# Optimization experiments

Hardware: AMD Instinct MI355X
Metric: run time of the kernel (lower is better)

## Reference

```python
import jax, jax.numpy as jnp
import numpy as np
import math

D_MODEL = 1024
NUM_HEADS = 16
HEAD_DIM = D_MODEL // NUM_HEADS
BLOCK_SIZE = 64
THRESHOLD = 0.99


def setup_inputs() -> dict:
    key = jax.random.key(0)
    ks = jax.random.split(key, 12)
    B, S, D = 2, 2048, D_MODEL
    scale = 1.0 / math.sqrt(D)
    x = jax.random.normal(ks[0], (B, S, D), dtype=jnp.float32)
    G_ii = jax.random.uniform(ks[1], (B, S), dtype=jnp.float32)
    # Linear weights stored as [in, out]; applied as x @ W + b (matches nn.Linear math).
    Wq = jax.random.normal(ks[2], (D, D), dtype=jnp.float32) * scale
    bq = jnp.zeros((D,), dtype=jnp.float32)
    Wk = jax.random.normal(ks[3], (D, D), dtype=jnp.float32) * scale
    bk = jnp.zeros((D,), dtype=jnp.float32)
    Wv = jax.random.normal(ks[4], (D, D), dtype=jnp.float32) * scale
    bv = jnp.zeros((D,), dtype=jnp.float32)
    Wo = jax.random.normal(ks[5], (D, D), dtype=jnp.float32) * scale
    bo = jnp.zeros((D,), dtype=jnp.float32)
    return {"x": x, "G_ii": G_ii, "Wq": Wq, "bq": bq, "Wk": Wk, "bk": bk,
            "Wv": Wv, "bv": bv, "Wo": Wo, "bo": bo}


def reference(x, G_ii, Wq, bq, Wk, bk, Wv, bv, Wo, bo):
    B, S, D = x.shape
    H, hd, bs = NUM_HEADS, HEAD_DIM, BLOCK_SIZE
    nb = S // bs

    # Projections and head split: [B, H, S, hd]
    q = (x @ Wq + bq).reshape(B, S, H, hd).transpose(0, 2, 1, 3)
    k = (x @ Wk + bk).reshape(B, S, H, hd).transpose(0, 2, 1, 3)
    v = (x @ Wv + bv).reshape(B, S, H, hd).transpose(0, 2, 1, 3)

    # Per-query-block scattering energy keep mask: block kept iff max |G_ii| >= threshold
    energy = jnp.abs(G_ii)                              # [B, S]
    block_max = energy.reshape(B, nb, bs).max(axis=-1)  # [B, nb]
    keep = (block_max >= THRESHOLD)                     # [B, nb] bool
    row_keep = jnp.repeat(keep, bs, axis=1)             # [B, S]

    # Kept query blocks attend densely (non-causal) over all keys; skipped blocks output zero.
    scores = jnp.einsum('bhqd,bhkd->bhqk', q, k) / math.sqrt(hd)  # [B, H, S, S]
    attn = jax.nn.softmax(scores, axis=-1)
    out = jnp.einsum('bhqk,bhkd->bhqd', attn, v)                  # [B, H, S, hd]
    out = out * row_keep[:, None, :, None].astype(out.dtype)

    out = out.transpose(0, 2, 1, 3).reshape(B, S, D)
    return out @ Wo + bo
```

## Files before the change

kernel.cpp:

```cpp
#include <hip/hip_runtime.h>
#include <math.h>

#define D_MODEL   1024
#define NUM_HEADS 16
#define HEAD_DIM  64
#define BS        64
#define NB        32
#define S_LEN     2048
#define BATCH     2
#define M_ROWS    (BATCH * S_LEN)
#define THRESH    0.99f
#define SCEXP     0.18033688f
#define NPH       (BATCH * NB * NUM_HEADS)
#define SPLITK    4

typedef __attribute__((ext_vector_type(8))) short bf16x8;
typedef __attribute__((ext_vector_type(8))) _Float16 f16x8;
typedef __attribute__((ext_vector_type(2))) __fp16 fp16v2;
typedef __attribute__((ext_vector_type(4))) float f32x4;

__device__ __forceinline__ unsigned short f2bf(float f) {
    unsigned int u = __float_as_uint(f);
    u += 0x7fff + ((u >> 16) & 1);
    return (unsigned short)(u >> 16);
}

__device__ __forceinline__ unsigned int pkrtz(float a, float b) {
    fp16v2 r = __builtin_amdgcn_cvt_pkrtz(a, b);
    return __builtin_bit_cast(unsigned int, r);
}

__device__ __forceinline__ void gload16(const void* gptr, void* lptr) {
    __builtin_amdgcn_global_load_lds(
        (const __attribute__((address_space(1))) void*)gptr,
        (__attribute__((address_space(3))) void*)lptr, 16, 0, 0);
}

__global__ __launch_bounds__(256) void prep_kernel(
    const float* __restrict__ x, const float* __restrict__ G,
    const float* __restrict__ Wq, const float* __restrict__ Wk,
    const float* __restrict__ Wv, const float* __restrict__ Wo,
    unsigned short* __restrict__ xb, unsigned short* __restrict__ wcat,
    unsigned short* __restrict__ wot, int* __restrict__ keep, int* __restrict__ work)
{
    const int bid = blockIdx.x, tid = threadIdx.x;
    __shared__ float T[64][65];

    if (bid < 2048) {
        size_t i = ((size_t)bid * 256 + tid) * 8;
        float4 a = *(const float4*)(x + i);
        float4 b = *(const float4*)(x + i + 4);
        uint4 o;
        o.x = (unsigned int)f2bf(a.x) | ((unsigned int)f2bf(a.y) << 16);
        o.y = (unsigned int)f2bf(a.z) | ((unsigned int)f2bf(a.w) << 16);
        o.z = (unsigned int)f2bf(b.x) | ((unsigned int)f2bf(b.y) << 16);
        o.w = (unsigned int)f2bf(b.z) | ((unsigned int)f2bf(b.w) << 16);
        *(uint4*)(xb + i) = o;
    } else if (bid < 3072) {
        int i = bid - 2048;
        int mat = i >> 8, rem = i & 255;
        int k0 = (rem & 15) * 64, n0 = (rem >> 4) * 64;
        const float* W = (mat == 0) ? Wq : (mat == 1) ? Wk : (mat == 2) ? Wv : Wo;
        int rr = tid >> 4, c4 = (tid & 15) * 4;
        #pragma unroll
        for (int j = 0; j < 4; j++) {
            int row = rr + j * 16;
            float4 v = *(const float4*)(W + (size_t)(k0 + row) * 1024 + n0 + c4);
            T[row][c4 + 0] = v.x; T[row][c4 + 1] = v.y;
            T[row][c4 + 2] = v.z; T[row][c4 + 3] = v.w;
        }
        __syncthreads();
        unsigned short* dst = (mat < 3) ? (wcat + (size_t)mat * 1024 * 1024) : wot;
        #pragma unroll
        for (int j = 0; j < 4; j++) {
            int n = rr + j * 16;
            unsigned int lo = (unsigned int)f2bf(T[c4 + 0][n]) | ((unsigned int)f2bf(T[c4 + 1][n]) << 16);
            unsigned int hi = (unsigned int)f2bf(T[c4 + 2][n]) | ((unsigned int)f2bf(T[c4 + 3][n]) << 16);
            *(uint2*)(dst + (size_t)(n0 + n) * 1024 + k0 + c4) = make_uint2(lo, hi);
        }
    } else {
        if (tid < 64) {
            int t = tid;
            const float4* g = (const float4*)(G + (size_t)t * 64);
            float mx = 0.f;
            #pragma unroll
            for (int j = 0; j < 16; j++) {
                float4 v = g[j];
                mx = fmaxf(mx, fmaxf(fmaxf(fabsf(v.x), fabsf(v.y)), fmaxf(fabsf(v.z), fabsf(v.w))));
            }
            bool k = (mx >= THRESH);
            unsigned long long bal = __ballot(k);
            int nk = __popcll(bal);
            unsigned long long below = bal & ((1ull << t) - 1ull);
            int nbelow = (int)__popcll(below);
            keep[t] = k ? 1 : 0;
            if (t == 0) work[0] = nk;
            int pos = k ? nbelow : (nk + t - nbelow);
            work[1 + pos] = t;
        }
    }
}

__global__ __launch_bounds__(256, 3) void gemm_qkv(
    const unsigned short* __restrict__ A, const unsigned short* __restrict__ Bt,
    const float* __restrict__ bq, const float* __restrict__ bk, const float* __restrict__ bv,
    const int* __restrict__ keep, unsigned short* __restrict__ qk, unsigned short* __restrict__ vt)
{
    const int n0 = blockIdx.x * 128, m0 = blockIdx.y * 128;
    const int tid = threadIdx.x, w = tid >> 6, lane = tid & 63;
    const int quad = lane >> 4, l16 = lane & 15;
    const int wm = w >> 1, wn = w & 1;
    const int kindb = n0 >> 10;
    if (kindb == 0 && !(keep[2 * blockIdx.y] | keep[2 * blockIdx.y + 1])) return;

    __shared__ union {
        struct { unsigned short As[2][128 * 32]; unsigned short Bs[2][128 * 32]; } s;
        unsigned short qkr[128 * 136];
        unsigned short vr[128 * 136];
    } u;

    f32x4 acc[4][4];
    #pragma unroll
    for (int mt = 0; mt < 4; mt++)
        #pragma unroll
        for (int nt = 0; nt < 4; nt++) acc[mt][nt] = (f32x4){0.f, 0.f, 0.f, 0.f};

    #define QSTAGE(it_, p_)                                                             \
        {                                                                               \
            int k0_ = (it_) * 32;                                                       \
            _Pragma("unroll")                                                           \
            for (int j = 0; j < 2; j++) {                                               \
                int s_ = w * 128 + j * 64 + lane; int row = s_ >> 2, cl = s_ & 3;       \
                int c = cl ^ ((row >> 1) & 3);                                          \
                gload16(A + (size_t)(m0 + row) * 1024 + k0_ + c * 8,                    \
                        &u.s.As[p_][(w * 128 + j * 64) * 8]);                           \
            }                                                                           \
            _Pragma("unroll")                                                           \
            for (int j = 0; j < 2; j++) {                                               \
                int s_ = w * 128 + j * 64 + lane; int row = s_ >> 2, cl = s_ & 3;       \
                int c = cl ^ ((row >> 1) & 3);                                          \
                gload16(Bt + (size_t)(n0 + row) * 1024 + k0_ + c * 8,                   \
                        &u.s.Bs[p_][(w * 128 + j * 64) * 8]);                           \
            }                                                                           \
        }

    QSTAGE(0, 0)

    for (int it = 0; it < 32; it++) {
        const int p = it & 1;
        __syncthreads();
        if (it + 1 < 32) QSTAGE(it + 1, (it + 1) & 1)

        bf16x8 af[4], bfr[4];
        #pragma unroll
        for (int mt = 0; mt < 4; mt++) {
            int row = wm * 64 + mt * 16 + l16;
            int cl = quad ^ ((row >> 1) & 3);
            af[mt] = *(const bf16x8*)&u.s.As[p][(row * 4 + cl) * 8];
        }
        #pragma unroll
        for (int nt = 0; nt < 4; nt++) {
            int row = wn * 64 + nt * 16 + l16;
            int cl = quad ^ ((row >> 1) & 3);
            bfr[nt] = *(const bf16x8*)&u.s.Bs[p][(row * 4 + cl) * 8];
        }
        #pragma unroll
        for (int mt = 0; mt < 4; mt++)
            #pragma unroll
            for (int nt = 0; nt < 4; nt++)
                acc[mt][nt] = __builtin_amdgcn_mfma_f32_16x16x32_bf16(af[mt], bfr[nt], acc[mt][nt], 0, 0, 0);
    }
    __syncthreads();

    if (kindb < 2) {
        const float* bp = (kindb == 0) ? bq : bk;
        const float sc = (kindb == 0) ? SCEXP : 1.0f;
        #pragma unroll
        for (int nt = 0; nt < 4; nt++) {
            int coll = wn * 64 + nt * 16 + l16;
            float bb = bp[(n0 & 1023) + coll];
            #pragma unroll
            for (int mt = 0; mt < 4; mt++)
                #pragma unroll
                for (int r = 0; r < 4; r++) {
                    int row = wm * 64 + mt * 16 + quad * 4 + r;
                    u.qkr[row * 136 + coll] = f2bf((acc[mt][nt][r] + bb) * sc);
                }
        }
        __syncthreads();
        #pragma unroll
        for (int i = 0; i < 8; i++) {
            int s_ = tid + i * 256;
            int row = s_ >> 4, c16 = s_ & 15;
            uint4 v = *(const uint4*)&u.qkr[row * 136 + c16 * 8];
            *(uint4*)(qk + (size_t)(m0 + row) * 2048 + n0 + c16 * 8) = v;
        }
    } else {
        #pragma unroll
        for (int nt = 0; nt < 4; nt++) {
            int coll = wn * 64 + nt * 16 + l16;
            float bb = bv[(n0 - 2048) + coll];
            #pragma unroll
            for (int mt = 0; mt < 4; mt++) {
                int s0 = wm * 64 + mt * 16 + quad * 4;
                uint2 pv;
                pv.x = pkrtz(acc[mt][nt][0] + bb, acc[mt][nt][1] + bb);
                pv.y = pkrtz(acc[mt][nt][2] + bb, acc[mt][nt][3] + bb);
                *(uint2*)&u.vr[coll * 136 + s0] = pv;
            }
        }
        __syncthreads();
        const int b_ = m0 >> 11, sbase = m0 & 2047;
        #pragma unroll
        for (int i = 0; i < 8; i++) {
            int s_ = tid + i * 256;
            int coll = s_ >> 4, ch = s_ & 15;
            uint4 v = *(const uint4*)&u.vr[coll * 136 + ch * 8];
            int colg = n0 - 2048 + coll;
            int h_ = colg >> 6, d = colg & 63;
            *(uint4*)(vt + ((size_t)(b_ * NUM_HEADS + h_) * HEAD_DIM + d) * 2048 + sbase + ch * 8) = v;
        }
    }
}

__global__ __launch_bounds__(256, 4) void gemm_out(
    const unsigned short* __restrict__ A, const unsigned short* __restrict__ Bt,
    const float* __restrict__ bo, const int* __restrict__ keep, float* __restrict__ out)
{
    const int n0 = blockIdx.x * 64, m0 = blockIdx.y * 64;
    const int tid = threadIdx.x, w = tid >> 6, lane = tid & 63;
    const int quad = lane >> 4, l16 = lane & 15;
    const int wm = w >> 1, wn = w & 1;

    if (!keep[blockIdx.y]) {
        #pragma unroll
        for (int i = 0; i < 4; i++) {
            int s_ = tid + i * 256;
            int row = s_ >> 4, c = (s_ & 15) * 4;
            *(float4*)(out + (size_t)(m0 + row) * 1024 + n0 + c) = *(const float4*)(bo + n0 + c);
        }
        return;
    }

    __shared__ unsigned short Asl[2][64 * 32];
    __shared__ unsigned short Bsl[2][64 * 32];

    f32x4 acc[2][2];
    #pragma unroll
    for (int mt = 0; mt < 2; mt++)
        #pragma unroll
        for (int nt = 0; nt < 2; nt++) acc[mt][nt] = (f32x4){0.f, 0.f, 0.f, 0.f};

    #define OSTAGE(it_, p_)                                                             \
        {                                                                               \
            int k0_ = (it_) * 32;                                                       \
            int s_ = w * 64 + lane; int row = s_ >> 2, cl = s_ & 3;                     \
            int c = cl ^ ((row >> 1) & 3);                                              \
            gload16(A  + (size_t)(m0 + row) * 1024 + k0_ + c * 8, &Asl[p_][(w * 64) * 8]); \
            gload16(Bt + (size_t)(n0 + row) * 1024 + k0_ + c * 8, &Bsl[p_][(w * 64) * 8]); \
        }

    OSTAGE(0, 0)

    for (int it = 0; it < 32; it++) {
        const int p = it & 1;
        __syncthreads();
        if (it + 1 < 32) OSTAGE(it + 1, (it + 1) & 1)

        bf16x8 af[2], bfr[2];
        #pragma unroll
        for (int mt = 0; mt < 2; mt++) {
            int row = wm * 32 + mt * 16 + l16;
            int cl = quad ^ ((row >> 1) & 3);
            af[mt] = *(const bf16x8*)&Asl[p][(row * 4 + cl) * 8];
        }
        #pragma unroll
        for (int nt = 0; nt < 2; nt++) {
            int row = wn * 32 + nt * 16 + l16;
            int cl = quad ^ ((row >> 1) & 3);
            bfr[nt] = *(const bf16x8*)&Bsl[p][(row * 4 + cl) * 8];
        }
        #pragma unroll
        for (int mt = 0; mt < 2; mt++)
            #pragma unroll
            for (int nt = 0; nt < 2; nt++)
                acc[mt][nt] = __builtin_amdgcn_mfma_f32_16x16x32_bf16(af[mt], bfr[nt], acc[mt][nt], 0, 0, 0);
    }

    #pragma unroll
    for (int nt = 0; nt < 2; nt++) {
        int col = n0 + wn * 32 + nt * 16 + l16;
        float bb = bo[col];
        #pragma unroll
        for (int mt = 0; mt < 2; mt++) {
            int mb = m0 + wm * 32 + mt * 16 + quad * 4;
            #pragma unroll
            for (int r = 0; r < 4; r++)
                out[(size_t)(mb + r) * 1024 + col] = acc[mt][nt][r] + bb;
        }
    }
}

__global__ __launch_bounds__(256, 4) void attn_kernel(
    const unsigned short* __restrict__ qk, const unsigned short* __restrict__ Vtg,
    const int* __restrict__ work,
    unsigned short* __restrict__ opart, float* __restrict__ lpart)
{
    const int bx = blockIdx.x, half = blockIdx.y;
    const int pair = bx >> 4, h = bx & 15;
    const int tid  = threadIdx.x;
    const int w    = tid >> 6, lane = tid & 63;
    const int quad = lane >> 4, l16 = lane & 15;

    if (pair >= work[0]) return;
    const int e = work[1 + pair];
    const int b = e >> 5, qblk = e & 31;

    __shared__ unsigned short Kbuf[2][BS * HEAD_DIM];
    __shared__ unsigned short Vbuf[2][HEAD_DIM * BS];
    __shared__ unsigned short Pt[4][16 * 64];

    const int KEYS = S_LEN / SPLITK;
    const int NCH  = KEYS / BS;
    const unsigned short* Qb = qk + (size_t)(b * S_LEN) * 2048 + h * 64;
    const unsigned short* Kb = qk + (size_t)(b * S_LEN + half * KEYS) * 2048 + 1024 + h * 64;
    const unsigned short* Vb = Vtg + (size_t)(b * NUM_HEADS + h) * HEAD_DIM * 2048 + half * KEYS;

    const int qrow = qblk * BS + w * 16 + l16;
    bf16x8 qf[2];
    #pragma unroll
    for (int ks = 0; ks < 2; ks++)
        qf[ks] = *(const bf16x8*)(Qb + (size_t)qrow * 2048 + ks * 32 + quad * 8);

    f32x4 o[4];
    #pragma unroll
    for (int mt = 0; mt < 4; mt++) o[mt] = (f32x4){0.f, 0.f, 0.f, 0.f};
    float l = 0.f;

    const int sA = w * 128 + lane, sB = sA + 64;
    const int rA = sA >> 3, cA = (sA & 7) ^ (rA & 7);
    const int rB = sB >> 3, cB = (sB & 7) ^ (rB & 7);
    const size_t koA = (size_t)rA * 2048 + cA * 8, koB = (size_t)rB * 2048 + cB * 8;

    uint4 kr0, kr1, vr0, vr1;
    #define LOADREGS(kc_)                                                       \
        {                                                                       \
            const unsigned short* kg_ = Kb + (size_t)(kc_) * BS * 2048;         \
            const unsigned short* vg_ = Vb + (size_t)(kc_) * BS;                \
            kr0 = *(const uint4*)(kg_ + koA); kr1 = *(const uint4*)(kg_ + koB); \
            vr0 = *(const uint4*)(vg_ + koA); vr1 = *(const uint4*)(vg_ + koB); \
        }
    #define WRITELDS(pb_)                                                       \
        {                                                                       \
            *(uint4*)&Kbuf[pb_][(size_t)sA * 8] = kr0;                          \
            *(uint4*)&Kbuf[pb_][(size_t)sB * 8] = kr1;                          \
            *(uint4*)&Vbuf[pb_][(size_t)sA * 8] = vr0;                          \
            *(uint4*)&Vbuf[pb_][(size_t)sB * 8] = vr1;                          \
        }

    LOADREGS(0)
    WRITELDS(0)
    __syncthreads();

    #pragma unroll
    for (int kc = 0; kc < NCH; kc++) {
        const int p = kc & 1;
        if (kc + 1 < NCH) LOADREGS(kc + 1)

        f32x4 st[4];
        #pragma unroll
        for (int mt = 0; mt < 4; mt++) {
            f32x4 acc = {0.f, 0.f, 0.f, 0.f};
            #pragma unroll
            for (int ks = 0; ks < 2; ks++) {
                int kk = mt * 16 + l16;
                bf16x8 kf = *(const bf16x8*)&Kbuf[p][(size_t)(kk * 8 + ((ks * 4 + quad) ^ (kk & 7))) * 8];
                acc = __builtin_amdgcn_mfma_f32_16x16x32_bf16(kf, qf[ks], acc, 0, 0, 0);
            }
            st[mt] = acc;
        }

        float pv[16], sum = 0.f;
        #pragma unroll
        for (int mt = 0; mt < 4; mt++)
            #pragma unroll
            for (int r = 0; r < 4; r++) {
                float ex = exp2f(st[mt][r]);
                pv[mt * 4 + r] = ex; sum += ex;
            }
        sum += __shfl_xor(sum, 16, 64);
        sum += __shfl_xor(sum, 32, 64);
        l += sum;

        #pragma unroll
        for (int mt = 0; mt < 4; mt++) {
            unsigned int lo = pkrtz(pv[mt * 4 + 0], pv[mt * 4 + 1]);
            unsigned int hi = pkrtz(pv[mt * 4 + 2], pv[mt * 4 + 3]);
            int c16 = 2 * mt + (quad >> 1);
            *(uint2*)&Pt[w][l16 * 64 + ((c16 ^ (l16 & 7)) * 8 + (quad & 1) * 4)] = make_uint2(lo, hi);
        }

        #pragma unroll
        for (int ks = 0; ks < 2; ks++) {
            f16x8 pf = *(const f16x8*)&Pt[w][l16 * 64 + (((4 * ks + quad) ^ (l16 & 7)) * 8)];
            #pragma unroll
            for (int mt = 0; mt < 4; mt++) {
                int d = mt * 16 + l16;
                f16x8 vf = *(const f16x8*)&Vbuf[p][(size_t)(d * 8 + ((ks * 4 + quad) ^ (d & 7))) * 8];
                o[mt] = __builtin_amdgcn_mfma_f32_16x16x32_f16(vf, pf, o[mt], 0, 0, 0);
            }
        }

        if (kc + 1 < NCH) {
            WRITELDS(p ^ 1)
            __syncthreads();
        }
    }

    unsigned short* ob = opart + ((size_t)(half * NPH + bx)) * 4096 + tid * 16;
    uint4 w0, w1;
    w0.x = pkrtz(o[0][0], o[0][1]); w0.y = pkrtz(o[0][2], o[0][3]);
    w0.z = pkrtz(o[1][0], o[1][1]); w0.w = pkrtz(o[1][2], o[1][3]);
    w1.x = pkrtz(o[2][0], o[2][1]); w1.y = pkrtz(o[2][2], o[2][3]);
    w1.z = pkrtz(o[3][0], o[3][1]); w1.w = pkrtz(o[3][2], o[3][3]);
    *(uint4*)ob = w0;
    *(uint4*)(ob + 8) = w1;
    if (quad == 0) lpart[(size_t)(half * NPH + bx) * 64 + w * 16 + l16] = l;
}

__global__ __launch_bounds__(256) void attn_combine(
    const unsigned short* __restrict__ opart, const float* __restrict__ lpart,
    const int* __restrict__ work, unsigned short* __restrict__ attn_out)
{
    const int bx = blockIdx.x;
    const int pair = bx >> 4, h = bx & 15;
    const int tid  = threadIdx.x;
    const int w    = tid >> 6, lane = tid & 63;
    const int quad = lane >> 4, l16 = lane & 15;

    const int e = work[1 + pair];
    const int b = e >> 5, qblk = e & 31;
    unsigned short* ablk = attn_out + ((size_t)(b * S_LEN + qblk * BS)) * D_MODEL + h * HEAD_DIM;

    if (pair >= work[0]) {
        uint4 z = make_uint4(0, 0, 0, 0);
        #pragma unroll
        for (int i = 0; i < 2; i++) {
            int u = tid + i * 256;
            int row = u >> 3, c8 = (u & 7) * 8;
            *(uint4*)(ablk + (size_t)row * D_MODEL + c8) = z;
        }
        return;
    }

    __shared__ float Obuf[4][HEAD_DIM * 17];

    float osum[16];
    #pragma unroll
    for (int j = 0; j < 16; j++) osum[j] = 0.f;
    float lsum = 0.f;
    #pragma unroll
    for (int hf = 0; hf < SPLITK; hf++) {
        const f16x8* pp = (const f16x8*)(opart + ((size_t)hf * NPH + bx) * 4096 + tid * 16);
        f16x8 a0 = pp[0], a1 = pp[1];
        #pragma unroll
        for (int j = 0; j < 8; j++) {
            osum[j]     += (float)a0[j];
            osum[8 + j] += (float)a1[j];
        }
        lsum += lpart[((size_t)hf * NPH + bx) * 64 + w * 16 + l16];
    }
    float inv = 1.0f / lsum;

    #pragma unroll
    for (int mt = 0; mt < 4; mt++)
        #pragma unroll
        for (int r = 0; r < 4; r++)
            Obuf[w][(mt * 16 + quad * 4 + r) * 17 + l16] = osum[mt * 4 + r] * inv;
    #pragma unroll
    for (int i = 0; i < 4; i++) {
        int uu = lane + 64 * i;
        int row = uu >> 4, d4 = (uu & 15) * 4;
        float x0 = Obuf[w][(d4 + 0) * 17 + row];
        float x1 = Obuf[w][(d4 + 1) * 17 + row];
        float x2 = Obuf[w][(d4 + 2) * 17 + row];
        float x3 = Obuf[w][(d4 + 3) * 17 + row];
        unsigned int lo = (unsigned int)f2bf(x0) | ((unsigned int)f2bf(x1) << 16);
        unsigned int hi = (unsigned int)f2bf(x2) | ((unsigned int)f2bf(x3) << 16);
        *(uint2*)(ablk + (size_t)(w * 16 + row) * D_MODEL + d4) = make_uint2(lo, hi);
    }
}

extern "C" void kernel_launch(void* const* d_in, const int* in_sizes, int n_in,
                              void* d_out, int out_size, void* d_ws, size_t ws_size,
                              hipStream_t stream) {
    const float* x  = (const float*)d_in[0];
    const float* G  = (const float*)d_in[1];
    const float* Wq = (const float*)d_in[2];
    const float* bq = (const float*)d_in[3];
    const float* Wk = (const float*)d_in[4];
    const float* bk = (const float*)d_in[5];
    const float* Wv = (const float*)d_in[6];
    const float* bv = (const float*)d_in[7];
    const float* Wo = (const float*)d_in[8];
    const float* bo = (const float*)d_in[9];
    float* out = (float*)d_out;

    char* wsp = (char*)d_ws;
    int* keep = (int*)wsp;
    int* work = keep + 64;
    unsigned short* xb    = (unsigned short*)(wsp + 1024);
    unsigned short* wcat  = xb + (size_t)M_ROWS * D_MODEL;
    unsigned short* wot   = wcat + (size_t)3 * 1024 * 1024;
    unsigned short* qk    = wot + (size_t)1024 * 1024;
    unsigned short* vt    = qk + (size_t)M_ROWS * 2048;
    unsigned short* attnb = vt + (size_t)BATCH * NUM_HEADS * HEAD_DIM * 2048;
    unsigned short* opart = attnb + (size_t)M_ROWS * D_MODEL;
    float* lpart = (float*)(opart + (size_t)SPLITK * NPH * 4096);

    prep_kernel<<<3073, 256, 0, stream>>>(x, G, Wq, Wk, Wv, Wo, xb, wcat, wot, keep, work);

    gemm_qkv<<<dim3(3072 / 128, M_ROWS / 128), 256, 0, stream>>>(
        xb, wcat, bq, bk, bv, keep, qk, vt);

    attn_kernel<<<dim3(NPH, SPLITK), 256, 0, stream>>>(qk, vt, work, opart, lpart);
    attn_combine<<<NPH, 256, 0, stream>>>(opart, lpart, work, attnb);

    gemm_out<<<dim3(1024 / 64, M_ROWS / 64), 256, 0, stream>>>(attnb, wot, bo, keep, out);
}
```

Measured before the change: 186.3 us.

## Software-pipeline QK^T one chunk ahead of softmax-PV in attention kernel

Restructures the attention inner loop so the QK^T MFMA for chunk i+1 is issued before the softmax and PV for chunk i. K and V loads and LDS writes are staggered separately so K runs two chunks ahead and V one chunk ahead. The change also adds s_setprio around the MFMA sections and swaps exp2f for the raw hardware exp2 builtin. The aim is to overlap exp and softmax ALU work with matrix-core work and to hide global load latency, at the cost of more live registers for the second score buffer.

```diff
diff --git a/kernel.cpp b/kernel.cpp
--- a/kernel.cpp
+++ b/kernel.cpp
@@ -343,79 +343,100 @@
     const size_t koA = (size_t)rA * 2048 + cA * 8, koB = (size_t)rB * 2048 + cB * 8;
 
     uint4 kr0, kr1, vr0, vr1;
-    #define LOADREGS(kc_)                                                       \
+    #define LOADK(kc_)                                                          \
         {                                                                       \
             const unsigned short* kg_ = Kb + (size_t)(kc_) * BS * 2048;         \
+            kr0 = *(const uint4*)(kg_ + koA); kr1 = *(const uint4*)(kg_ + koB); \
+        }
+    #define LOADV(kc_)                                                          \
+        {                                                                       \
             const unsigned short* vg_ = Vb + (size_t)(kc_) * BS;                \
-            kr0 = *(const uint4*)(kg_ + koA); kr1 = *(const uint4*)(kg_ + koB); \
             vr0 = *(const uint4*)(vg_ + koA); vr1 = *(const uint4*)(vg_ + koB); \
         }
-    #define WRITELDS(pb_)                                                       \
+    #define WRITEK(pb_)                                                         \
         {                                                                       \
             *(uint4*)&Kbuf[pb_][(size_t)sA * 8] = kr0;                          \
             *(uint4*)&Kbuf[pb_][(size_t)sB * 8] = kr1;                          \
+        }
+    #define WRITEV(pb_)                                                         \
+        {                                                                       \
             *(uint4*)&Vbuf[pb_][(size_t)sA * 8] = vr0;                          \
             *(uint4*)&Vbuf[pb_][(size_t)sB * 8] = vr1;                          \
         }
-
-    LOADREGS(0)
-    WRITELDS(0)
+    #define QKT(pb_, st_)                                                                        \
+        {                                                                                        \
+            __builtin_amdgcn_s_setprio(1);                                                       \
+            _Pragma("unroll")                                                                    \
+            for (int mt = 0; mt < 4; mt++) {                                                     \
+                f32x4 a_ = {0.f, 0.f, 0.f, 0.f};                                                 \
+                _Pragma("unroll")                                                                \
+                for (int ks = 0; ks < 2; ks++) {                                                 \
+                    int kk = mt * 16 + l16;                                                      \
+                    bf16x8 kf = *(const bf16x8*)&Kbuf[pb_][(size_t)(kk * 8 + ((ks * 4 + quad) ^ (kk & 7))) * 8]; \
+                    a_ = __builtin_amdgcn_mfma_f32_16x16x32_bf16(kf, qf[ks], a_, 0, 0, 0);       \
+                }                                                                                \
+                st_[mt] = a_;                                                                    \
+            }                                                                                    \
+            __builtin_amdgcn_s_setprio(0);                                                       \
+        }
+    #define SMPV(st_, pbv_)                                                                      \
+        {                                                                                        \
+            float pvv[16], sum = 0.f;                                                            \
+            _Pragma("unroll")                                                                    \
+            for (int mt = 0; mt < 4; mt++)                                                       \
+                _Pragma("unroll")                                                                \
+                for (int r = 0; r < 4; r++) {                                                    \
+                    float ex = __builtin_amdgcn_exp2f(st_[mt][r]);                               \
+                    pvv[mt * 4 + r] = ex; sum += ex;                                             \
+                }                                                                                \
+            sum += __shfl_xor(sum, 16, 64);                                                      \
+            sum += __shfl_xor(sum, 32, 64);                                                      \
+            l += sum;                                                                            \
+            _Pragma("unroll")                                                                    \
+            for (int mt = 0; mt < 4; mt++) {                                                     \
+                unsigned int lo = pkrtz(pvv[mt * 4 + 0], pvv[mt * 4 + 1]);                       \
+                unsigned int hi = pkrtz(pvv[mt * 4 + 2], pvv[mt * 4 + 3]);                       \
+                int c16 = 2 * mt + (quad >> 1);                                                  \
+                *(uint2*)&Pt[w][l16 * 64 + ((c16 ^ (l16 & 7)) * 8 + (quad & 1) * 4)] = make_uint2(lo, hi); \
+            }                                                                                    \
+            __builtin_amdgcn_s_setprio(1);                                                       \
+            _Pragma("unroll")                                                                    \
+            for (int ks = 0; ks < 2; ks++) {                                                     \
+                f16x8 pf = *(const f16x8*)&Pt[w][l16 * 64 + (((4 * ks + quad) ^ (l16 & 7)) * 8)];\
+                _Pragma("unroll")                                                                \
+                for (int mt = 0; mt < 4; mt++) {                                                 \
+                    int d = mt * 16 + l16;                                                       \
+                    f16x8 vf = *(const f16x8*)&Vbuf[pbv_][(size_t)(d * 8 + ((ks * 4 + quad) ^ (d & 7))) * 8]; \
+                    o[mt] = __builtin_amdgcn_mfma_f32_16x16x32_f16(vf, pf, o[mt], 0, 0, 0);      \
+                }                                                                                \
+            }                                                                                    \
+            __builtin_amdgcn_s_setprio(0);                                                       \
+        }
+
+    LOADK(0) LOADV(0)
+    WRITEK(0) WRITEV(0)
+    LOADK(1)
     __syncthreads();
 
-    #pragma unroll
-    for (int kc = 0; kc < NCH; kc++) {
-        const int p = kc & 1;
-        if (kc + 1 < NCH) LOADREGS(kc + 1)
-
-        f32x4 st[4];
-        #pragma unroll
-        for (int mt = 0; mt < 4; mt++) {
-            f32x4 acc = {0.f, 0.f, 0.f, 0.f};
-            #pragma unroll
-            for (int ks = 0; ks < 2; ks++) {
-                int kk = mt * 16 + l16;
-                bf16x8 kf = *(const bf16x8*)&Kbuf[p][(size_t)(kk * 8 + ((ks * 4 + quad) ^ (kk & 7))) * 8];
-                acc = __builtin_amdgcn_mfma_f32_16x16x32_bf16(kf, qf[ks], acc, 0, 0, 0);
-            }
-            st[mt] = acc;
-        }
-
-        float pv[16], sum = 0.f;
-        #pragma unroll
-        for (int mt = 0; mt < 4; mt++)
-            #pragma unroll
-            for (int r = 0; r < 4; r++) {
-                float ex = exp2f(st[mt][r]);
-                pv[mt * 4 + r] = ex; sum += ex;
-            }
-        sum += __shfl_xor(sum, 16, 64);
-        sum += __shfl_xor(sum, 32, 64);
-        l += sum;
-
-        #pragma unroll
-        for (int mt = 0; mt < 4; mt++) {
-            unsigned int lo = pkrtz(pv[mt * 4 + 0], pv[mt * 4 + 1]);
-            unsigned int hi = pkrtz(pv[mt * 4 + 2], pv[mt * 4 + 3]);
-            int c16 = 2 * mt + (quad >> 1);
-            *(uint2*)&Pt[w][l16 * 64 + ((c16 ^ (l16 & 7)) * 8 + (quad & 1) * 4)] = make_uint2(lo, hi);
-        }
-
-        #pragma unroll
-        for (int ks = 0; ks < 2; ks++) {
-            f16x8 pf = *(const f16x8*)&Pt[w][l16 * 64 + (((4 * ks + quad) ^ (l16 & 7)) * 8)];
-            #pragma unroll
-            for (int mt = 0; mt < 4; mt++) {
-                int d = mt * 16 + l16;
-                f16x8 vf = *(const f16x8*)&Vbuf[p][(size_t)(d * 8 + ((ks * 4 + quad) ^ (d & 7))) * 8];
-                o[mt] = __builtin_amdgcn_mfma_f32_16x16x32_f16(vf, pf, o[mt], 0, 0, 0);
-            }
-        }
-
-        if (kc + 1 < NCH) {
-            WRITELDS(p ^ 1)
-            __syncthreads();
-        }
-    }
+    f32x4 st0[4], st1[4];
+    QKT(0, st0)
+    WRITEK(1)
+    LOADK(2) LOADV(1)
+    __syncthreads();
+
+    #pragma unroll
+    for (int i = 0; i < NCH - 1; i++) {
+        QKT((i + 1) & 1, st1)
+        SMPV(st0, i & 1)
+        if (i + 2 < NCH) WRITEK(i & 1)
+        WRITEV((i + 1) & 1)
+        if (i + 3 < NCH) LOADK(i + 3)
+        if (i + 2 < NCH) LOADV(i + 2)
+        __syncthreads();
+        #pragma unroll
+        for (int mt = 0; mt < 4; mt++) st0[mt] = st1[mt];
+    }
+    SMPV(st0, (NCH - 1) & 1)
 
     unsigned short* ob = opart + ((size_t)(half * NPH + bx)) * 4096 + tid * 16;
     uint4 w0, w1;
```

After: 191.7 us. +2.9%, slower.

## Process two kept query blocks per attention workgroup to share K/V tiles

Applied to the files above, without the earlier changes.

The work list is rebuilt so kept query blocks are paired within each batch, padded with a duplicate when the count is odd, and skipped and dummy slots are flagged. Each attention workgroup now computes two query blocks against the same staged K/V chunk, halving K/V global loads and LDS staging per query block and doubling MFMA work per load. It also uses the raw exp2 intrinsic and raises wave priority around the MFMA sections. The cost is more registers (occupancy hint lowered from 4 to 3), wasted work on padded pairs, and more complex slot indexing in the combine kernel.

```diff
diff --git a/kernel.cpp b/kernel.cpp
--- a/kernel.cpp
+++ b/kernel.cpp
@@ -11,8 +11,9 @@
 #define M_ROWS    (BATCH * S_LEN)
 #define THRESH    0.99f
 #define SCEXP     0.18033688f
-#define NPH       (BATCH * NB * NUM_HEADS)
 #define SPLITK    4
+#define NSLOT     66
+#define SLOTB     (NSLOT * 16)
 
 typedef __attribute__((ext_vector_type(8))) short bf16x8;
 typedef __attribute__((ext_vector_type(8))) _Float16 f16x8;
@@ -90,13 +91,27 @@
             }
             bool k = (mx >= THRESH);
             unsigned long long bal = __ballot(k);
-            int nk = __popcll(bal);
-            unsigned long long below = bal & ((1ull << t) - 1ull);
-            int nbelow = (int)__popcll(below);
+            unsigned int mk0 = (unsigned int)bal, mk1 = (unsigned int)(bal >> 32);
+            int nk0 = __popc(mk0), nk1 = __popc(mk1);
+            int ND0 = (nk0 + 1) >> 1, ND1 = (nk1 + 1) >> 1;
             keep[t] = k ? 1 : 0;
-            if (t == 0) work[0] = nk;
-            int pos = k ? nbelow : (nk + t - nbelow);
-            work[1 + pos] = t;
+            int tb = t & 31, bb = t >> 5;
+            unsigned int mb = bb ? mk1 : mk0;
+            unsigned int msk = (tb == 0) ? 0u : ((1u << tb) - 1u);
+            int rank = __popc(mb & msk);
+            int rd   = __popc(~mb & msk);
+            int base = bb ? 2 * ND0 : 0;
+            int dbase = 2 * ND0 + 2 * ND1;
+            int doff = bb ? (32 - nk0) : 0;
+            if (k)  work[1 + base + rank] = t;
+            else    work[1 + dbase + doff + rd] = t | (1 << 8);
+            if (t == 0) {
+                work[0] = ND0 + ND1;
+                if (nk0 & 1) work[1 + nk0] = (31 - __clz(mk0)) | (2 << 8);
+                if (nk1 & 1) work[1 + 2 * ND0 + nk1] = (63 - __clz(mk1)) | (2 << 8);
+                int total = dbase + (64 - nk0 - nk1);
+                for (int j = total; j < NSLOT; j++) work[1 + j] = (2 << 8);
+            }
         }
     }
 }
@@ -301,24 +316,25 @@
     }
 }
 
-__global__ __launch_bounds__(256, 4) void attn_kernel(
+__global__ __launch_bounds__(256, 3) void attn_kernel(
     const unsigned short* __restrict__ qk, const unsigned short* __restrict__ Vtg,
     const int* __restrict__ work,
     unsigned short* __restrict__ opart, float* __restrict__ lpart)
 {
     const int bx = blockIdx.x, half = blockIdx.y;
-    const int pair = bx >> 4, h = bx & 15;
+    const int dpair = bx >> 4, h = bx & 15;
     const int tid  = threadIdx.x;
     const int w    = tid >> 6, lane = tid & 63;
     const int quad = lane >> 4, l16 = lane & 15;
 
-    if (pair >= work[0]) return;
-    const int e = work[1 + pair];
-    const int b = e >> 5, qblk = e & 31;
+    if (dpair >= work[0]) return;
+    const int j0 = 2 * dpair, j1 = j0 + 1;
+    const int t0 = work[1 + j0] & 63, t1 = work[1 + j1] & 63;
+    const int b = t0 >> 5, qb0 = t0 & 31, qb1 = t1 & 31;
 
     __shared__ unsigned short Kbuf[2][BS * HEAD_DIM];
     __shared__ unsigned short Vbuf[2][HEAD_DIM * BS];
-    __shared__ unsigned short Pt[4][16 * 64];
+    __shared__ unsigned short Pt[4][2][16 * 64];
 
     const int KEYS = S_LEN / SPLITK;
     const int NCH  = KEYS / BS;
@@ -326,16 +342,19 @@
     const unsigned short* Kb = qk + (size_t)(b * S_LEN + half * KEYS) * 2048 + 1024 + h * 64;
     const unsigned short* Vb = Vtg + (size_t)(b * NUM_HEADS + h) * HEAD_DIM * 2048 + half * KEYS;
 
-    const int qrow = qblk * BS + w * 16 + l16;
-    bf16x8 qf[2];
-    #pragma unroll
-    for (int ks = 0; ks < 2; ks++)
-        qf[ks] = *(const bf16x8*)(Qb + (size_t)qrow * 2048 + ks * 32 + quad * 8);
-
-    f32x4 o[4];
-    #pragma unroll
-    for (int mt = 0; mt < 4; mt++) o[mt] = (f32x4){0.f, 0.f, 0.f, 0.f};
-    float l = 0.f;
+    const int qrow0 = qb0 * BS + w * 16 + l16;
+    const int qrow1 = qb1 * BS + w * 16 + l16;
+    bf16x8 qf0[2], qf1[2];
+    #pragma unroll
+    for (int ks = 0; ks < 2; ks++) {
+        qf0[ks] = *(const bf16x8*)(Qb + (size_t)qrow0 * 2048 + ks * 32 + quad * 8);
+        qf1[ks] = *(const bf16x8*)(Qb + (size_t)qrow1 * 2048 + ks * 32 + quad * 8);
+    }
+
+    f32x4 o0[4], o1[4];
+    #pragma unroll
+    for (int mt = 0; mt < 4; mt++) { o0[mt] = (f32x4){0.f,0.f,0.f,0.f}; o1[mt] = (f32x4){0.f,0.f,0.f,0.f}; }
+    float l0 = 0.f, l1 = 0.f;
 
     const int sA = w * 128 + lane, sB = sA + 64;
     const int rA = sA >> 3, cA = (sA & 7) ^ (rA & 7);
@@ -367,49 +386,61 @@
         const int p = kc & 1;
         if (kc + 1 < NCH) LOADREGS(kc + 1)
 
-        f32x4 st[4];
+        f32x4 st0[4], st1[4];
+        __builtin_amdgcn_s_setprio(1);
         #pragma unroll
         for (int mt = 0; mt < 4; mt++) {
-            f32x4 acc = {0.f, 0.f, 0.f, 0.f};
+            f32x4 a0 = {0.f,0.f,0.f,0.f}, a1 = {0.f,0.f,0.f,0.f};
             #pragma unroll
             for (int ks = 0; ks < 2; ks++) {
                 int kk = mt * 16 + l16;
                 bf16x8 kf = *(const bf16x8*)&Kbuf[p][(size_t)(kk * 8 + ((ks * 4 + quad) ^ (kk & 7))) * 8];
-                acc = __builtin_amdgcn_mfma_f32_16x16x32_bf16(kf, qf[ks], acc, 0, 0, 0);
+                a0 = __builtin_amdgcn_mfma_f32_16x16x32_bf16(kf, qf0[ks], a0, 0, 0, 0);
+                a1 = __builtin_amdgcn_mfma_f32_16x16x32_bf16(kf, qf1[ks], a1, 0, 0, 0);
             }
-            st[mt] = acc;
-        }
-
-        float pv[16], sum = 0.f;
-        #pragma unroll
-        for (int mt = 0; mt < 4; mt++)
-            #pragma unroll
-            for (int r = 0; r < 4; r++) {
-                float ex = exp2f(st[mt][r]);
-                pv[mt * 4 + r] = ex; sum += ex;
-            }
-        sum += __shfl_xor(sum, 16, 64);
-        sum += __shfl_xor(sum, 32, 64);
-        l += sum;
-
+            st0[mt] = a0; st1[mt] = a1;
+        }
+        __builtin_amdgcn_s_setprio(0);
+
+        float sum0 = 0.f, sum1 = 0.f;
         #pragma unroll
         for (int mt = 0; mt < 4; mt++) {
-            unsigned int lo = pkrtz(pv[mt * 4 + 0], pv[mt * 4 + 1]);
-            unsigned int hi = pkrtz(pv[mt * 4 + 2], pv[mt * 4 + 3]);
             int c16 = 2 * mt + (quad >> 1);
-            *(uint2*)&Pt[w][l16 * 64 + ((c16 ^ (l16 & 7)) * 8 + (quad & 1) * 4)] = make_uint2(lo, hi);
-        }
-
+            int off = (c16 ^ (l16 & 7)) * 8 + (quad & 1) * 4;
+            float e00 = __builtin_amdgcn_exp2f(st0[mt][0]);
+            float e01 = __builtin_amdgcn_exp2f(st0[mt][1]);
+            float e02 = __builtin_amdgcn_exp2f(st0[mt][2]);
+            float e03 = __builtin_amdgcn_exp2f(st0[mt][3]);
+            sum0 += (e00 + e01) + (e02 + e03);
+            *(uint2*)&Pt[w][0][l16 * 64 + off] = make_uint2(pkrtz(e00, e01), pkrtz(e02, e03));
+            float e10 = __builtin_amdgcn_exp2f(st1[mt][0]);
+            float e11 = __builtin_amdgcn_exp2f(st1[mt][1]);
+            float e12 = __builtin_amdgcn_exp2f(st1[mt][2]);
+            float e13 = __builtin_amdgcn_exp2f(st1[mt][3]);
+            sum1 += (e10 + e11) + (e12 + e13);
+            *(uint2*)&Pt[w][1][l16 * 64 + off] = make_uint2(pkrtz(e10, e11), pkrtz(e12, e13));
+        }
+        sum0 += __shfl_xor(sum0, 16, 64);
+        sum0 += __shfl_xor(sum0, 32, 64);
+        sum1 += __shfl_xor(sum1, 16, 64);
+        sum1 += __shfl_xor(sum1, 32, 64);
+        l0 += sum0; l1 += sum1;
+
+        __builtin_amdgcn_s_setprio(1);
         #pragma unroll
         for (int ks = 0; ks < 2; ks++) {
-            f16x8 pf = *(const f16x8*)&Pt[w][l16 * 64 + (((4 * ks + quad) ^ (l16 & 7)) * 8)];
+            int poff = ((4 * ks + quad) ^ (l16 & 7)) * 8;
+            f16x8 pf0 = *(const f16x8*)&Pt[w][0][l16 * 64 + poff];
+            f16x8 pf1 = *(const f16x8*)&Pt[w][1][l16 * 64 + poff];
             #pragma unroll
             for (int mt = 0; mt < 4; mt++) {
                 int d = mt * 16 + l16;
                 f16x8 vf = *(const f16x8*)&Vbuf[p][(size_t)(d * 8 + ((ks * 4 + quad) ^ (d & 7))) * 8];
-                o[mt] = __builtin_amdgcn_mfma_f32_16x16x32_f16(vf, pf, o[mt], 0, 0, 0);
+                o0[mt] = __builtin_amdgcn_mfma_f32_16x16x32_f16(vf, pf0, o0[mt], 0, 0, 0);
+                o1[mt] = __builtin_amdgcn_mfma_f32_16x16x32_f16(vf, pf1, o1[mt], 0, 0, 0);
             }
         }
+        __builtin_amdgcn_s_setprio(0);
 
         if (kc + 1 < NCH) {
             WRITELDS(p ^ 1)
@@ -417,15 +448,30 @@
         }
     }
 
-    unsigned short* ob = opart + ((size_t)(half * NPH + bx)) * 4096 + tid * 16;
-    uint4 w0, w1;
-    w0.x = pkrtz(o[0][0], o[0][1]); w0.y = pkrtz(o[0][2], o[0][3]);
-    w0.z = pkrtz(o[1][0], o[1][1]); w0.w = pkrtz(o[1][2], o[1][3]);
-    w1.x = pkrtz(o[2][0], o[2][1]); w1.y = pkrtz(o[2][2], o[2][3]);
-    w1.z = pkrtz(o[3][0], o[3][1]); w1.w = pkrtz(o[3][2], o[3][3]);
-    *(uint4*)ob = w0;
-    *(uint4*)(ob + 8) = w1;
-    if (quad == 0) lpart[(size_t)(half * NPH + bx) * 64 + w * 16 + l16] = l;
+    {
+        unsigned short* ob = opart + ((size_t)(half * SLOTB + j0 * 16 + h)) * 4096 + tid * 16;
+        uint4 w0, w1;
+        w0.x = pkrtz(o0[0][0], o0[0][1]); w0.y = pkrtz(o0[0][2], o0[0][3]);
+        w0.z = pkrtz(o0[1][0], o0[1][1]); w0.w = pkrtz(o0[1][2], o0[1][3]);
+        w1.x = pkrtz(o0[2][0], o0[2][1]); w1.y = pkrtz(o0[2][2], o0[2][3]);
+        w1.z = pkrtz(o0[3][0], o0[3][1]); w1.w = pkrtz(o0[3][2], o0[3][3]);
+        *(uint4*)ob = w0;
+        *(uint4*)(ob + 8) = w1;
+    }
+    {
+        unsigned short* ob = opart + ((size_t)(half * SLOTB + j1 * 16 + h)) * 4096 + tid * 16;
+        uint4 w0, w1;
+        w0.x = pkrtz(o1[0][0], o1[0][1]); w0.y = pkrtz(o1[0][2], o1[0][3]);
+        w0.z = pkrtz(o1[1][0], o1[1][1]); w0.w = pkrtz(o1[1][2], o1[1][3]);
+        w1.x = pkrtz(o1[2][0], o1[2][1]); w1.y = pkrtz(o1[2][2], o1[2][3]);
+        w1.z = pkrtz(o1[3][0], o1[3][1]); w1.w = pkrtz(o1[3][2], o1[3][3]);
+        *(uint4*)ob = w0;
+        *(uint4*)(ob + 8) = w1;
+    }
+    if (quad == 0) {
+        lpart[((size_t)half * SLOTB + j0 * 16 + h) * 64 + w * 16 + l16] = l0;
+        lpart[((size_t)half * SLOTB + j1 * 16 + h) * 64 + w * 16 + l16] = l1;
+    }
 }
 
 __global__ __launch_bounds__(256) void attn_combine(
@@ -439,10 +485,12 @@
     const int quad = lane >> 4, l16 = lane & 15;
 
     const int e = work[1 + pair];
-    const int b = e >> 5, qblk = e & 31;
+    const int flag = e >> 8, t = e & 63;
+    if (flag == 2) return;
+    const int b = t >> 5, qblk = t & 31;
     unsigned short* ablk = attn_out + ((size_t)(b * S_LEN + qblk * BS)) * D_MODEL + h * HEAD_DIM;
 
-    if (pair >= work[0]) {
+    if (flag == 1) {
         uint4 z = make_uint4(0, 0, 0, 0);
         #pragma unroll
         for (int i = 0; i < 2; i++) {
@@ -461,14 +509,14 @@
     float lsum = 0.f;
     #pragma unroll
     for (int hf = 0; hf < SPLITK; hf++) {
-        const f16x8* pp = (const f16x8*)(opart + ((size_t)hf * NPH + bx) * 4096 + tid * 16);
+        const f16x8* pp = (const f16x8*)(opart + ((size_t)hf * SLOTB + bx) * 4096 + tid * 16);
         f16x8 a0 = pp[0], a1 = pp[1];
         #pragma unroll
         for (int j = 0; j < 8; j++) {
             osum[j]     += (float)a0[j];
             osum[8 + j] += (float)a1[j];
         }
-        lsum += lpart[((size_t)hf * NPH + bx) * 64 + w * 16 + l16];
+        lsum += lpart[((size_t)hf * SLOTB + bx) * 64 + w * 16 + l16];
     }
     float inv = 1.0f / lsum;
 
@@ -516,15 +564,15 @@
     unsigned short* vt    = qk + (size_t)M_ROWS * 2048;
     unsigned short* attnb = vt + (size_t)BATCH * NUM_HEADS * HEAD_DIM * 2048;
     unsigned short* opart = attnb + (size_t)M_ROWS * D_MODEL;
-    float* lpart = (float*)(opart + (size_t)SPLITK * NPH * 4096);
+    float* lpart = (float*)(opart + (size_t)SPLITK * SLOTB * 4096);
 
     prep_kernel<<<3073, 256, 0, stream>>>(x, G, Wq, Wk, Wv, Wo, xb, wcat, wot, keep, work);
 
     gemm_qkv<<<dim3(3072 / 128, M_ROWS / 128), 256, 0, stream>>>(
         xb, wcat, bq, bk, bv, keep, qk, vt);
 
-    attn_kernel<<<dim3(NPH, SPLITK), 256, 0, stream>>>(qk, vt, work, opart, lpart);
-    attn_combine<<<NPH, 256, 0, stream>>>(opart, lpart, work, attnb);
+    attn_kernel<<<dim3(32 * 16, SPLITK), 256, 0, stream>>>(qk, vt, work, opart, lpart);
+    attn_combine<<<SLOTB, 256, 0, stream>>>(opart, lpart, work, attnb);
 
     gemm_out<<<dim3(1024 / 64, M_ROWS / 64), 256, 0, stream>>>(attnb, wot, bo, keep, out);
 }
```

After: 178.4 us. 4.2% less time.
